# Kernel optimization log

Hardware: AMD Instinct MI355X
Metric: run time of the kernel (lower is better)

Reference implementation:

```python
import jax, jax.numpy as jnp
import numpy as np


def setup_inputs() -> dict:
    key = jax.random.key(0)
    ks = jax.random.split(key, 13)
    B, C, H, W = 1, 72, 64, 64
    nc, cs = 18, 4  # num_chunks, chunk_size (teacher_dim=72, student_dim=18)
    s = 0.1
    return {
        "x": jax.random.normal(ks[0], (B, C, H, W), jnp.float32),
        # per-chunk 1x1-conv QKV weights [nc, out=cs, in=cs] and biases [nc, cs]
        "Wq": jax.random.normal(ks[1], (nc, cs, cs), jnp.float32) * s,
        "bq": jax.random.normal(ks[2], (nc, cs), jnp.float32) * s,
        "Wk": jax.random.normal(ks[3], (nc, cs, cs), jnp.float32) * s,
        "bk": jax.random.normal(ks[4], (nc, cs), jnp.float32) * s,
        "Wv": jax.random.normal(ks[5], (nc, cs, cs), jnp.float32) * s,
        "bv": jax.random.normal(ks[6], (nc, cs), jnp.float32) * s,
        # global 1x1-conv QKV [C, C] and biases [C]
        "WqG": jax.random.normal(ks[7], (C, C), jnp.float32) * s,
        "bqG": jax.random.normal(ks[8], (C,), jnp.float32) * s,
        "WkG": jax.random.normal(ks[9], (C, C), jnp.float32) * s,
        "bkG": jax.random.normal(ks[10], (C,), jnp.float32) * s,
        "WvG": jax.random.normal(ks[11], (C, C), jnp.float32) * s,
        "bvG": jax.random.normal(ks[12], (C,), jnp.float32) * s,
    }


def reference(x, Wq, bq, Wk, bk, Wv, bv, WqG, bqG, WkG, bkG, WvG, bvG):
    B, C, H, W = x.shape
    nc, cs = Wq.shape[0], Wq.shape[1]
    N = H * W
    scale = 1.0 / np.sqrt(np.float32(N))

    # [B, nc, cs, N] chunked view of x
    xc = x.reshape(B, nc, cs, N)

    # per-chunk 1x1 conv == per-chunk channel mixing
    q = jnp.einsum('noi,bnip->bnop', Wq, xc) + bq[None, :, :, None]
    k = jnp.einsum('noi,bnip->bnop', Wk, xc) + bk[None, :, :, None]
    v = jnp.einsum('noi,bnip->bnop', Wv, xc) + bv[None, :, :, None]

    # attn[i,j] = (q^T k)[i,j] / sqrt(N), softmax over j
    scores = jnp.einsum('bnci,bncj->bnij', q, k) * scale  # [B,nc,N,N]
    attn = jax.nn.softmax(scores, axis=-1)
    # out[c,i] = sum_j v[c,j] * attn[j,i]  (v @ attn in torch)
    attended = jnp.einsum('bncj,bnji->bnci', v, attn)  # [B,nc,cs,N]

    # global attention over all C channels
    xf = x.reshape(B, C, N)
    qG = jnp.einsum('oc,bcp->bop', WqG, xf) + bqG[None, :, None]
    kG = jnp.einsum('oc,bcp->bop', WkG, xf) + bkG[None, :, None]
    vG = jnp.einsum('oc,bcp->bop', WvG, xf) + bvG[None, :, None]
    scoresG = jnp.einsum('bci,bcj->bij', qG, kG) * scale  # [B,N,N]
    attnG = jax.nn.softmax(scoresG, axis=-1)
    outG = jnp.einsum('bcj,bji->bci', vG, attnG).reshape(B, nc, cs, N)

    combined = attended + outG  # [B,nc,cs,N]
    pooled = jnp.sum(xc * combined, axis=2).reshape(B, nc, H, W)
    return pooled
```

## Files before the change

### kernel.cpp

```cpp
#include <hip/hip_runtime.h>

#define NPIX 4096
#define NCH 72
#define NCHUNK 18
#define KPAD 96

static constexpr float SCALE_LOG2E = 0.022542110013890054f;
static constexpr float SCALE_N = 0.015625f;

#define OFF_QC 0
#define OFF_KC 294912
#define OFF_VC 589824
#define OFF_VG 884736
#define OFF_DG 1179648
#define OFF_OUTG 1183744
#define OFF_QB 1478656
#define OFF_KB 1675264
#define OFF_WB 1871872
#define OFF_SM 2035712
#define OFF_WM 2036000
#define WS_FLOATS 2037152

typedef __attribute__((ext_vector_type(8))) short short8v;
typedef __attribute__((ext_vector_type(4))) float f32x4;

__device__ __forceinline__ float fexp2(float x) {
#if __has_builtin(__builtin_amdgcn_exp2f)
  return __builtin_amdgcn_exp2f(x);
#else
  return exp2f(x);
#endif
}

__device__ __forceinline__ unsigned short bf16r(float f) {
  unsigned int u = __float_as_uint(f);
  u = (u + 0x7FFFu + ((u >> 16) & 1u)) >> 16;
  return (unsigned short)u;
}
__device__ __forceinline__ unsigned int bf16pair(float lo, float hi) {
  return (unsigned int)bf16r(lo) | ((unsigned int)bf16r(hi) << 16);
}

__device__ __forceinline__ f32x4 MFMA(short8v a, short8v b, f32x4 c) {
  return __builtin_amdgcn_mfma_f32_16x16x32_bf16(a, b, c, 0, 0, 0);
}

__device__ __forceinline__ float dot4(float4 a, float4 b) {
  return a.x*b.x + a.y*b.y + a.z*b.z + a.w*b.w;
}

__device__ __forceinline__ float4 mix4(const float* __restrict__ W, const float* __restrict__ b,
                                       float x0, float x1, float x2, float x3, float sc)
{
  float4 r;
  r.x = (b[0] + W[0]*x0  + W[1]*x1  + W[2]*x2  + W[3]*x3)  * sc;
  r.y = (b[1] + W[4]*x0  + W[5]*x1  + W[6]*x2  + W[7]*x3)  * sc;
  r.z = (b[2] + W[8]*x0  + W[9]*x1  + W[10]*x2 + W[11]*x3) * sc;
  r.w = (b[3] + W[12]*x0 + W[13]*x1 + W[14]*x2 + W[15]*x3) * sc;
  return r;
}

__global__ __launch_bounds__(256, 3) void k_qkv(const float* __restrict__ x,
    const float* __restrict__ Wq, const float* __restrict__ bq,
    const float* __restrict__ Wk, const float* __restrict__ bk,
    const float* __restrict__ Wv, const float* __restrict__ bv,
    const float* __restrict__ WqG, const float* __restrict__ bqG,
    const float* __restrict__ WkG, const float* __restrict__ bkG,
    const float* __restrict__ WvG, const float* __restrict__ bvG,
    float* __restrict__ ws)
{
  const int p = blockIdx.x * blockDim.x + threadIdx.x;
  const int seg = blockIdx.y;
  if (seg < 6) {
    float4* qd = reinterpret_cast<float4*>(ws + OFF_QC);
    float4* kd = reinterpret_cast<float4*>(ws + OFF_KC);
    float4* vd = reinterpret_cast<float4*>(ws + OFF_VC);
    const int n0 = seg * 3;
#pragma unroll
    for (int dn = 0; dn < 3; ++dn) {
      const int n = n0 + dn;
      const float x0 = x[(4*n+0)*NPIX + p];
      const float x1 = x[(4*n+1)*NPIX + p];
      const float x2 = x[(4*n+2)*NPIX + p];
      const float x3 = x[(4*n+3)*NPIX + p];
      float4 q = mix4(Wq + n*16, bq + n*4, x0, x1, x2, x3, SCALE_N);
      float4 k = mix4(Wk + n*16, bk + n*4, x0, x1, x2, x3, 1.0f);
      float4 v = mix4(Wv + n*16, bv + n*4, x0, x1, x2, x3, 1.0f);
      qd[(size_t)n*NPIX + p] = q;
      kd[(size_t)n*NPIX + p] = k;
      vd[(size_t)n*NPIX + p] = v;
    }
  } else {
    const int m = (seg - 6) / 6;
    const int g6 = (seg - 6) % 6;
    const float* W = (m == 0) ? WqG : (m == 1) ? WkG : WvG;
    const float* b = (m == 0) ? bqG : (m == 1) ? bkG : bvG;
    float4 xv[18];
#pragma unroll
    for (int c = 0; c < 18; ++c) {
      float4 t;
      t.x = x[(4*c+0)*NPIX + p];
      t.y = x[(4*c+1)*NPIX + p];
      t.z = x[(4*c+2)*NPIX + p];
      t.w = x[(4*c+3)*NPIX + p];
      xv[c] = t;
    }
    const int ob = g6 * 12;
    if (m == 2) {
      float* dst = ws + OFF_VG;
      for (int o = ob; o < ob + 12; ++o) {
        float acc = b[o];
        const float4* wrow = reinterpret_cast<const float4*>(W + o*NCH);
#pragma unroll
        for (int c = 0; c < 18; ++c) acc += dot4(wrow[c], xv[c]);
        dst[o*NPIX + p] = acc;
      }
    } else {
      unsigned short* dst = reinterpret_cast<unsigned short*>(ws + ((m == 0) ? OFF_QB : OFF_KB));
      const float sc = (m == 0) ? SCALE_LOG2E : 1.0f;
      for (int o = ob; o < ob + 12; ++o) {
        float acc = b[o];
        const float4* wrow = reinterpret_cast<const float4*>(W + o*NCH);
#pragma unroll
        for (int c = 0; c < 18; ++c) acc += dot4(wrow[c], xv[c]);
        dst[p*KPAD + o] = bf16r(acc * sc);
      }
      if (g6 == 5) {
#pragma unroll
        for (int o = NCH; o < KPAD; ++o) dst[p*KPAD + o] = 0;
      }
    }
  }
}

__global__ __launch_bounds__(256, 4) void k_kmom(float* __restrict__ ws)
{
  const int n = blockIdx.y;
  const int tid = threadIdx.x;
  const float4* kc = reinterpret_cast<const float4*>(ws + OFF_KC) + (size_t)n*NPIX + blockIdx.x*1024;
  float f[14];
#pragma unroll
  for (int i = 0; i < 14; ++i) f[i] = 0.f;
#pragma unroll
  for (int s = 0; s < 4; ++s) {
    float4 k = kc[s*256 + tid];
    f[0] += k.x; f[1] += k.y; f[2] += k.z; f[3] += k.w;
    f[4] += 0.5f*k.x*k.x; f[5] += k.x*k.y; f[6]  += k.x*k.z; f[7]  += k.x*k.w;
    f[8] += 0.5f*k.y*k.y; f[9] += k.y*k.z; f[10] += k.y*k.w;
    f[11] += 0.5f*k.z*k.z; f[12] += k.z*k.w; f[13] += 0.5f*k.w*k.w;
  }
#pragma unroll
  for (int m = 1; m < 64; m <<= 1) {
#pragma unroll
    for (int i = 0; i < 14; ++i) f[i] += __shfl_xor(f[i], m, 64);
  }
  if ((tid & 63) == 0) {
    float* SM = ws + OFF_SM + n*16;
#pragma unroll
    for (int i = 0; i < 14; ++i) atomicAdd(&SM[i], f[i]);
  }
}

__global__ __launch_bounds__(256, 4) void k_cmom(float* __restrict__ ws)
{
  const int n = blockIdx.y;
  const int tid = threadIdx.x;
  const size_t base = (size_t)n*NPIX + blockIdx.x*1024;
  const float4* qc = reinterpret_cast<const float4*>(ws + OFF_QC) + base;
  const float4* vc = reinterpret_cast<const float4*>(ws + OFF_VC) + base;
  const float* SM = ws + OFF_SM + n*16;
  const float s10 = SM[0], s11 = SM[1], s12 = SM[2], s13 = SM[3];
  float s2[10];
#pragma unroll
  for (int i = 0; i < 10; ++i) s2[i] = SM[4+i];
  float mom[60];
#pragma unroll
  for (int i = 0; i < 60; ++i) mom[i] = 0.f;
#pragma unroll
  for (int s = 0; s < 4; ++s) {
    float4 q = qc[s*256 + tid];
    float4 v = vc[s*256 + tid];
    float P[10];
    P[0] = q.x*q.x; P[1] = q.x*q.y; P[2] = q.x*q.z; P[3] = q.x*q.w;
    P[4] = q.y*q.y; P[5] = q.y*q.z; P[6] = q.y*q.w;
    P[7] = q.z*q.z; P[8] = q.z*q.w; P[9] = q.w*q.w;
    float D = 4096.0f + s10*q.x + s11*q.y + s12*q.z + s13*q.w;
#pragma unroll
    for (int i = 0; i < 10; ++i) D += s2[i]*P[i];
    const float inv = 1.0f / D;
    const float wc[4] = { v.x*inv, v.y*inv, v.z*inv, v.w*inv };
    float F[15];
    F[0] = 1.f; F[1] = q.x; F[2] = q.y; F[3] = q.z; F[4] = q.w;
    F[5]  = 0.5f*P[0]; F[6]  = P[1]; F[7]  = P[2]; F[8] = P[3];
    F[9]  = 0.5f*P[4]; F[10] = P[5]; F[11] = P[6];
    F[12] = 0.5f*P[7]; F[13] = P[8]; F[14] = 0.5f*P[9];
#pragma unroll
    for (int c = 0; c < 4; ++c) {
#pragma unroll
      for (int i = 0; i < 15; ++i) mom[c*15 + i] += wc[c]*F[i];
    }
  }
#pragma unroll
  for (int m = 1; m < 64; m <<= 1) {
#pragma unroll
    for (int i = 0; i < 60; ++i) mom[i] += __shfl_xor(mom[i], m, 64);
  }
  if ((tid & 63) == 0) {
    float* WM = ws + OFF_WM + n*64;
#pragma unroll
    for (int i = 0; i < 60; ++i) atomicAdd(&WM[i], mom[i]);
  }
}

__global__ __launch_bounds__(256, 4) void k_mA(float* __restrict__ ws)
{
  const unsigned short* QB = reinterpret_cast<const unsigned short*>(ws + OFF_QB);
  const unsigned short* KB = reinterpret_cast<const unsigned short*>(ws + OFF_KB);
  const int w = threadIdx.x >> 6, l = threadIdx.x & 63;
  const int g = l >> 4, li = l & 15;
  const int j0 = blockIdx.x * 64 + w * 16;
  const int i0 = blockIdx.y * 256;
  short8v qa[3];
#pragma unroll
  for (int kk = 0; kk < 3; ++kk)
    qa[kk] = *reinterpret_cast<const short8v*>(QB + (j0 + li)*KPAD + kk*32 + 8*g);
  float ds0 = 0.f, ds1 = 0.f, ds2 = 0.f, ds3 = 0.f;
#pragma unroll 2
  for (int t = 0; t < 16; ++t) {
    const int i = i0 + t*16;
    f32x4 acc = {0.f, 0.f, 0.f, 0.f};
#pragma unroll
    for (int kk = 0; kk < 3; ++kk) {
      short8v kb = *reinterpret_cast<const short8v*>(KB + (i + li)*KPAD + kk*32 + 8*g);
      acc = MFMA(qa[kk], kb, acc);
    }
    ds0 += fexp2(acc[0]);
    ds1 += fexp2(acc[1]);
    ds2 += fexp2(acc[2]);
    ds3 += fexp2(acc[3]);
  }
#pragma unroll
  for (int m = 1; m < 16; m <<= 1) {
    ds0 += __shfl_xor(ds0, m, 64);
    ds1 += __shfl_xor(ds1, m, 64);
    ds2 += __shfl_xor(ds2, m, 64);
    ds3 += __shfl_xor(ds3, m, 64);
  }
  if (li == 0) {
    float* D = ws + OFF_DG;
    atomicAdd(&D[j0 + 4*g + 0], ds0);
    atomicAdd(&D[j0 + 4*g + 1], ds1);
    atomicAdd(&D[j0 + 4*g + 2], ds2);
    atomicAdd(&D[j0 + 4*g + 3], ds3);
  }
}

__global__ void k_wcompG(float* __restrict__ ws)
{
  const int j = blockIdx.x * blockDim.x + threadIdx.x;
  const float inv = 1.0f / ws[OFF_DG + j];
  unsigned short* WB = reinterpret_cast<unsigned short*>(ws + OFF_WB);
  const float* VG = ws + OFF_VG;
#pragma unroll
  for (int c = 0; c < NCH; ++c)
    WB[c*NPIX + j] = bf16r(VG[c*NPIX + j] * inv);
#pragma unroll
  for (int c = NCH; c < 80; ++c) WB[c*NPIX + j] = 0;
}

__global__ __launch_bounds__(256, 4) void k_mB(float* __restrict__ ws)
{
  __shared__ unsigned int E_dw[2][4][16][36];
  const unsigned short* QB = reinterpret_cast<const unsigned short*>(ws + OFF_QB);
  const unsigned short* KB = reinterpret_cast<const unsigned short*>(ws + OFF_KB);
  const unsigned short* WB = reinterpret_cast<const unsigned short*>(ws + OFF_WB);
  const int w = threadIdx.x >> 6, l = threadIdx.x & 63;
  const int g = l >> 4, li = l & 15;
  const int iw = blockIdx.x * 64 + w * 16;
  const int jbase = blockIdx.y * 256;
  short8v kb[3];
#pragma unroll
  for (int kk = 0; kk < 3; ++kk)
    kb[kk] = *reinterpret_cast<const short8v*>(KB + (iw + li)*KPAD + kk*32 + 8*g);
  f32x4 accW[5];
#pragma unroll
  for (int m = 0; m < 5; ++m) accW[m] = (f32x4){0.f, 0.f, 0.f, 0.f};
#pragma unroll 2
  for (int t = 0; t < 8; ++t) {
    const int jb = jbase + t*32;
    unsigned int (*Em)[36] = E_dw[t & 1][w];
#pragma unroll
    for (int m = 0; m < 2; ++m) {
      f32x4 acc = {0.f, 0.f, 0.f, 0.f};
#pragma unroll
      for (int kk = 0; kk < 3; ++kk) {
        short8v qa = *reinterpret_cast<const short8v*>(QB + (jb + m*16 + li)*KPAD + kk*32 + 8*g);
        acc = MFMA(qa, kb[kk], acc);
      }
      Em[li][m*8 + 2*g    ] = bf16pair(fexp2(acc[0]), fexp2(acc[1]));
      Em[li][m*8 + 2*g + 1] = bf16pair(fexp2(acc[2]), fexp2(acc[3]));
    }
    short8v eb = *reinterpret_cast<const short8v*>(&Em[li][4*g]);
#pragma unroll
    for (int m = 0; m < 5; ++m) {
      short8v wa = *reinterpret_cast<const short8v*>(WB + (m*16 + li)*NPIX + jb + 8*g);
      accW[m] = MFMA(wa, eb, accW[m]);
    }
  }
  float* OG = ws + OFF_OUTG;
#pragma unroll
  for (int m = 0; m < 5; ++m) {
#pragma unroll
    for (int r = 0; r < 4; ++r) {
      const int c = m*16 + 4*g + r;
      if (c < NCH) atomicAdd(&OG[c*NPIX + iw + li], accW[m][r]);
    }
  }
}

__global__ void k_final(const float* __restrict__ x, const float* __restrict__ ws,
                        float* __restrict__ out)
{
  const int n = blockIdx.x >> 4;
  const int p = ((blockIdx.x & 15) << 8) + threadIdx.x;
  const float4 k = reinterpret_cast<const float4*>(ws + OFF_KC)[(size_t)n*NPIX + p];
  const float* M = ws + OFF_WM + n*64;
  float P[10];
  P[0] = k.x*k.x; P[1] = k.x*k.y; P[2] = k.x*k.z; P[3] = k.x*k.w;
  P[4] = k.y*k.y; P[5] = k.y*k.z; P[6] = k.y*k.w;
  P[7] = k.z*k.z; P[8] = k.z*k.w; P[9] = k.w*k.w;
  const float* og = ws + OFF_OUTG + (size_t)n*4*NPIX + p;
  float s = 0.f;
#pragma unroll
  for (int c = 0; c < 4; ++c) {
    const float* mc = M + c*15;
    float oc = mc[0] + mc[1]*k.x + mc[2]*k.y + mc[3]*k.z + mc[4]*k.w;
#pragma unroll
    for (int i = 0; i < 10; ++i) oc += mc[5+i]*P[i];
    s += x[(4*n + c)*NPIX + p] * (oc + og[c*NPIX]);
  }
  out[n*NPIX + p] = s;
}

extern "C" void kernel_launch(void* const* d_in, const int* in_sizes, int n_in,
                              void* d_out, int out_size, void* d_ws, size_t ws_size,
                              hipStream_t stream)
{
  const float* x   = (const float*)d_in[0];
  const float* Wq  = (const float*)d_in[1];
  const float* bq  = (const float*)d_in[2];
  const float* Wk  = (const float*)d_in[3];
  const float* bk  = (const float*)d_in[4];
  const float* Wv  = (const float*)d_in[5];
  const float* bv  = (const float*)d_in[6];
  const float* WqG = (const float*)d_in[7];
  const float* bqG = (const float*)d_in[8];
  const float* WkG = (const float*)d_in[9];
  const float* bkG = (const float*)d_in[10];
  const float* WvG = (const float*)d_in[11];
  const float* bvG = (const float*)d_in[12];
  float* ws  = (float*)d_ws;
  float* out = (float*)d_out;

  if (ws_size < (size_t)WS_FLOATS * sizeof(float)) return;

  hipMemsetAsync(ws + OFF_DG, 0, (size_t)(4096 + NCH*NPIX) * sizeof(float), stream);
  hipMemsetAsync(ws + OFF_SM, 0, (size_t)(WS_FLOATS - OFF_SM) * sizeof(float), stream);

  hipLaunchKernelGGL(k_qkv, dim3(16, 24), dim3(256), 0, stream,
                     x, Wq, bq, Wk, bk, Wv, bv, WqG, bqG, WkG, bkG, WvG, bvG, ws);
  hipLaunchKernelGGL(k_kmom, dim3(4, 18), dim3(256), 0, stream, ws);
  hipLaunchKernelGGL(k_mA, dim3(64, 16), dim3(256), 0, stream, ws);
  hipLaunchKernelGGL(k_cmom, dim3(4, 18), dim3(256), 0, stream, ws);
  hipLaunchKernelGGL(k_wcompG, dim3(16), dim3(256), 0, stream, ws);
  hipLaunchKernelGGL(k_mB, dim3(64, 16), dim3(256), 0, stream, ws);
  hipLaunchKernelGGL(k_final, dim3(288), dim3(256), 0, stream, x, ws, out);
}
```

Baseline: 107.2 us.

## Split k_mB over j into four partial buffers, reduce in-block and drop atomics

k_mB is re-gridded so that each block handles 16 query rows, and its four waves each take a different 256-wide j slice inside one of four 1024-wide j segments. Wave partials are reduced through shared memory, then written with plain stores into four separate partial-output regions, reusing dead workspace buffers (QC, VC, VG). k_final now sums those four partials. This replaces 16-way float atomics and the large memset of the output accumulator with one extra sync, an LDS reduction and extra reads in the final kernel. It relies on QC, VC and VG being no longer needed once k_mB runs.

```diff
diff --git a/kernel.cpp b/kernel.cpp
--- a/kernel.cpp
+++ b/kernel.cpp
@@ -271,17 +271,19 @@
 __global__ __launch_bounds__(256, 4) void k_mB(float* __restrict__ ws)
 {
   __shared__ unsigned int E_dw[2][4][16][36];
+  __shared__ f32x4 red[3][64][5];
   const unsigned short* QB = reinterpret_cast<const unsigned short*>(ws + OFF_QB);
   const unsigned short* KB = reinterpret_cast<const unsigned short*>(ws + OFF_KB);
   const unsigned short* WB = reinterpret_cast<const unsigned short*>(ws + OFF_WB);
   const int w = threadIdx.x >> 6, l = threadIdx.x & 63;
   const int g = l >> 4, li = l & 15;
-  const int iw = blockIdx.x * 64 + w * 16;
-  const int jbase = blockIdx.y * 256;
+  const int i0 = blockIdx.x * 16;
+  const int s = blockIdx.y;
+  const int jbase = s * 1024 + w * 256;
   short8v kb[3];
 #pragma unroll
   for (int kk = 0; kk < 3; ++kk)
-    kb[kk] = *reinterpret_cast<const short8v*>(KB + (iw + li)*KPAD + kk*32 + 8*g);
+    kb[kk] = *reinterpret_cast<const short8v*>(KB + (i0 + li)*KPAD + kk*32 + 8*g);
   f32x4 accW[5];
 #pragma unroll
   for (int m = 0; m < 5; ++m) accW[m] = (f32x4){0.f, 0.f, 0.f, 0.f};
@@ -307,13 +309,25 @@
       accW[m] = MFMA(wa, eb, accW[m]);
     }
   }
-  float* OG = ws + OFF_OUTG;
-#pragma unroll
-  for (int m = 0; m < 5; ++m) {
-#pragma unroll
-    for (int r = 0; r < 4; ++r) {
-      const int c = m*16 + 4*g + r;
-      if (c < NCH) atomicAdd(&OG[c*NPIX + iw + li], accW[m][r]);
+  if (w > 0) {
+#pragma unroll
+    for (int m = 0; m < 5; ++m) red[w-1][l][m] = accW[m];
+  }
+  __syncthreads();
+  if (w == 0) {
+#pragma unroll
+    for (int o = 0; o < 3; ++o)
+#pragma unroll
+      for (int m = 0; m < 5; ++m) accW[m] += red[o][l][m];
+    const int pbase[4] = { OFF_QC, OFF_VC, OFF_VG, OFF_OUTG };
+    float* OP = ws + pbase[s];
+#pragma unroll
+    for (int m = 0; m < 5; ++m) {
+#pragma unroll
+      for (int r = 0; r < 4; ++r) {
+        const int c = m*16 + 4*g + r;
+        if (c < NCH) OP[(size_t)c*NPIX + i0 + li] = accW[m][r];
+      }
     }
   }
 }
@@ -329,7 +343,6 @@
   P[0] = k.x*k.x; P[1] = k.x*k.y; P[2] = k.x*k.z; P[3] = k.x*k.w;
   P[4] = k.y*k.y; P[5] = k.y*k.z; P[6] = k.y*k.w;
   P[7] = k.z*k.z; P[8] = k.z*k.w; P[9] = k.w*k.w;
-  const float* og = ws + OFF_OUTG + (size_t)n*4*NPIX + p;
   float s = 0.f;
 #pragma unroll
   for (int c = 0; c < 4; ++c) {
@@ -337,7 +350,10 @@
     float oc = mc[0] + mc[1]*k.x + mc[2]*k.y + mc[3]*k.z + mc[4]*k.w;
 #pragma unroll
     for (int i = 0; i < 10; ++i) oc += mc[5+i]*P[i];
-    s += x[(4*n + c)*NPIX + p] * (oc + og[c*NPIX]);
+    const size_t off = (size_t)(4*n + c)*NPIX + p;
+    const float og = ws[OFF_QC + off] + ws[OFF_VC + off]
+                   + ws[OFF_VG + off] + ws[OFF_OUTG + off];
+    s += x[off] * (oc + og);
   }
   out[n*NPIX + p] = s;
 }
@@ -364,7 +380,7 @@
 
   if (ws_size < (size_t)WS_FLOATS * sizeof(float)) return;
 
-  hipMemsetAsync(ws + OFF_DG, 0, (size_t)(4096 + NCH*NPIX) * sizeof(float), stream);
+  hipMemsetAsync(ws + OFF_DG, 0, (size_t)4096 * sizeof(float), stream);
   hipMemsetAsync(ws + OFF_SM, 0, (size_t)(WS_FLOATS - OFF_SM) * sizeof(float), stream);
 
   hipLaunchKernelGGL(k_qkv, dim3(16, 24), dim3(256), 0, stream,
@@ -373,6 +389,6 @@
   hipLaunchKernelGGL(k_mA, dim3(64, 16), dim3(256), 0, stream, ws);
   hipLaunchKernelGGL(k_cmom, dim3(4, 18), dim3(256), 0, stream, ws);
   hipLaunchKernelGGL(k_wcompG, dim3(16), dim3(256), 0, stream, ws);
-  hipLaunchKernelGGL(k_mB, dim3(64, 16), dim3(256), 0, stream, ws);
+  hipLaunchKernelGGL(k_mB, dim3(256, 4), dim3(256), 0, stream, ws);
   hipLaunchKernelGGL(k_final, dim3(288), dim3(256), 0, stream, x, ws, out);
 }
```

Result: faster. 103.4 us (-3.6%).
